# Kernel optimization log

Hardware: AMD Instinct MI355X
Metric: run time of the kernel (lower is better)

Reference implementation:

```python
import jax, jax.numpy as jnp
import numpy as np

CODEBOOK_SIZE = 8192
DIM = 64
B, N = 4, 4096


def setup_inputs() -> dict:
    key = jax.random.key(0)
    k1, k2 = jax.random.split(key)
    x = jax.random.normal(k1, (B, N, DIM), dtype=jnp.float32)
    node_mask = jnp.ones((B, N), dtype=jnp.float32)
    embed = jax.random.normal(k2, (CODEBOOK_SIZE, DIM), dtype=jnp.float32)
    return {"x": x, "node_mask": node_mask, "embed": embed}


def reference(x, node_mask, embed):
    # x: [B, N, D]; embed: [K, D]; node_mask: [B, N]
    b, n, d = x.shape
    k = embed.shape[0]
    flatten = x.reshape(-1, d)  # [B*N, D]
    dist = -(
        jnp.sum(flatten * flatten, axis=1, keepdims=True)
        - 2.0 * (flatten @ embed.T)
        + jnp.sum(embed * embed, axis=1)[None, :]
    )
    embed_ind = jnp.argmax(dist, axis=-1)  # [B*N] nearest-code assignment
    quantize = embed[embed_ind].reshape(b, n, d)  # codebook gather
    # masked one-hot stats (embed_onehot * node_mask), via segment_sum
    mask_flat = node_mask.reshape(-1)
    counts = jax.ops.segment_sum(mask_flat, embed_ind, num_segments=k)  # [K]
    avg_probs = counts / jnp.asarray(flatten.shape[0], dtype=x.dtype)
    perplexity = jnp.exp(-jnp.sum(avg_probs * jnp.log(avg_probs + 1e-10)))
    return quantize, embed_ind.reshape(b, n), perplexity
```

## Files before the change

### kernel.cpp

```cpp
#include <hip/hip_runtime.h>

typedef __attribute__((ext_vector_type(8))) short short8;
typedef __attribute__((ext_vector_type(4))) float f32x4;

#define ROWS 16384
#define DIM 64
#define NCODES 8192
#define MARGIN 0.008f
#define KT_FB 256
#define CTS_PER_BLOCK 32

#define WS_BEST   0
#define WS_COUNTS 131072
#define WS_ENH    163840
#define WS_ESWZ   196608
#define WS_NEED   2293760

__device__ __forceinline__ unsigned long long pack_score(float s, int idx) {
  unsigned u = __float_as_uint(s);
  u ^= (unsigned)((int)u >> 31) | 0x80000000u;
  return ((unsigned long long)u << 32) | (unsigned)(0xFFFF - idx);
}
__device__ __forceinline__ unsigned short bf16hi(float f) {
  unsigned u = __float_as_uint(f);
  return (unsigned short)((u + 0x7FFFu + ((u >> 16) & 1u)) >> 16);
}

__global__ void vq_enorm(const float* __restrict__ embed, float* __restrict__ enh) {
  int k = blockIdx.x * 256 + threadIdx.x;
  const float4* e4 = (const float4*)(embed + (size_t)k * DIM);
  float a = 0.f, b = 0.f, c = 0.f, d = 0.f;
#pragma unroll
  for (int i = 0; i < DIM / 4; ++i) {
    float4 v = e4[i];
    a = fmaf(v.x, v.x, a); b = fmaf(v.y, v.y, b);
    c = fmaf(v.z, v.z, c); d = fmaf(v.w, v.w, d);
  }
  enh[k] = 0.5f * ((a + b) + (c + d));
}

__global__ void vq_prep_e(const float* __restrict__ embed, short* __restrict__ eswz) {
  int u = blockIdx.x * 256 + threadIdx.x;
  int l = u & 63, kc = (u >> 6) & 1, ct = u >> 7;
  int code = ct * 16 + (l & 15);
  int kb = kc * 32 + (l >> 4) * 8;
  const float* er = embed + (size_t)code * DIM + kb;
  short8 h8, l8;
#pragma unroll
  for (int j = 0; j < 8; ++j) {
    float v = er[j];
    unsigned short h = bf16hi(v);
    float r = v - __uint_as_float((unsigned)h << 16);
    h8[j] = (short)h;
    l8[j] = (short)bf16hi(r);
  }
  short8* dst = (short8*)eswz;
  size_t frag = (size_t)(ct * 2 + kc) * 2;
  dst[(frag + 0) * 64 + l] = h8;
  dst[(frag + 1) * 64 + l] = l8;
}

__global__ __launch_bounds__(256, 4) void vq_screen(
    const float* __restrict__ x, const float* __restrict__ embed,
    const short* __restrict__ eswz, const float* __restrict__ enh,
    unsigned long long* __restrict__ best) {
  const int l = threadIdx.x & 63, wid = threadIdx.x >> 6;
  const int cl = l & 15, grp = l >> 4;
  const int row0 = blockIdx.x * 128 + wid * 32;
  const int ct0 = blockIdx.y * CTS_PER_BLOCK;

  short8 ahi[2][2], alo[2][2];
#pragma unroll
  for (int s = 0; s < 2; ++s) {
    const float* xr = x + (size_t)(row0 + s * 16 + cl) * DIM;
#pragma unroll
    for (int kc = 0; kc < 2; ++kc) {
      const int kb = kc * 32 + grp * 8;
#pragma unroll
      for (int j = 0; j < 8; ++j) {
        float v = xr[kb + j];
        unsigned short h = bf16hi(v);
        float r = v - __uint_as_float((unsigned)h << 16);
        ahi[s][kc][j] = (short)h;
        alo[s][kc][j] = (short)bf16hi(r);
      }
    }
  }

  const short8* eb = (const short8*)eswz;
  float bsc[2][4];
  int bidx[2][4];
#pragma unroll
  for (int s = 0; s < 2; ++s)
#pragma unroll
    for (int j = 0; j < 4; ++j) { bsc[s][j] = -3.4e38f; bidx[s][j] = 0; }

#pragma unroll 2
  for (int ct = ct0; ct < ct0 + CTS_PER_BLOCK; ++ct) {
    size_t f0 = (size_t)(ct * 2 + 0) * 128, f1 = (size_t)(ct * 2 + 1) * 128;
    short8 bh0 = eb[f0 + l], bl0 = eb[f0 + 64 + l];
    short8 bh1 = eb[f1 + l], bl1 = eb[f1 + 64 + l];
    float eh = enh[ct * 16 + cl];

    f32x4 accI = {-eh, -eh, -eh, -eh};
    f32x4 acc0 = accI, acc1 = accI;
    acc0 = __builtin_amdgcn_mfma_f32_16x16x32_bf16(ahi[0][0], bh0, acc0, 0, 0, 0);
    acc1 = __builtin_amdgcn_mfma_f32_16x16x32_bf16(ahi[1][0], bh0, acc1, 0, 0, 0);
    acc0 = __builtin_amdgcn_mfma_f32_16x16x32_bf16(alo[0][0], bh0, acc0, 0, 0, 0);
    acc1 = __builtin_amdgcn_mfma_f32_16x16x32_bf16(alo[1][0], bh0, acc1, 0, 0, 0);
    acc0 = __builtin_amdgcn_mfma_f32_16x16x32_bf16(ahi[0][0], bl0, acc0, 0, 0, 0);
    acc1 = __builtin_amdgcn_mfma_f32_16x16x32_bf16(ahi[1][0], bl0, acc1, 0, 0, 0);
    acc0 = __builtin_amdgcn_mfma_f32_16x16x32_bf16(ahi[0][1], bh1, acc0, 0, 0, 0);
    acc1 = __builtin_amdgcn_mfma_f32_16x16x32_bf16(ahi[1][1], bh1, acc1, 0, 0, 0);
    acc0 = __builtin_amdgcn_mfma_f32_16x16x32_bf16(alo[0][1], bh1, acc0, 0, 0, 0);
    acc1 = __builtin_amdgcn_mfma_f32_16x16x32_bf16(alo[1][1], bh1, acc1, 0, 0, 0);
    acc0 = __builtin_amdgcn_mfma_f32_16x16x32_bf16(ahi[0][1], bl1, acc0, 0, 0, 0);
    acc1 = __builtin_amdgcn_mfma_f32_16x16x32_bf16(ahi[1][1], bl1, acc1, 0, 0, 0);

    const int code = ct * 16 + cl;
#pragma unroll
    for (int j = 0; j < 4; ++j) {
      if (acc0[j] > bsc[0][j]) { bsc[0][j] = acc0[j]; bidx[0][j] = code; }
      if (acc1[j] > bsc[1][j]) { bsc[1][j] = acc1[j]; bidx[1][j] = code; }
    }
  }

  unsigned fmask = 0;
#pragma unroll
  for (int s = 0; s < 2; ++s)
#pragma unroll
    for (int j = 0; j < 4; ++j) {
      float m = bsc[s][j];
      m = fmaxf(m, __shfl_xor(m, 1));
      m = fmaxf(m, __shfl_xor(m, 2));
      m = fmaxf(m, __shfl_xor(m, 4));
      m = fmaxf(m, __shfl_xor(m, 8));
      if (bsc[s][j] >= m - MARGIN) fmask |= 1u << (s * 4 + j);
    }

  float exact[2][4];
#pragma unroll
  for (int s = 0; s < 2; ++s)
#pragma unroll
    for (int j = 0; j < 4; ++j) exact[s][j] = -3.4e38f;

  while (__any((int)(fmask != 0))) {
    const bool act = fmask != 0;
    const int sel = __ffs(fmask) - 1;
    int code = 0;
#pragma unroll
    for (int s = 0; s < 2; ++s)
#pragma unroll
      for (int j = 0; j < 4; ++j)
        code = (sel == s * 4 + j) ? bidx[s][j] : code;
    int row = act ? (row0 + (sel >> 2) * 16 + grp * 4 + (sel & 3)) : row0;
    if (!act) code = 0;
    const float4* xr = (const float4*)(x + (size_t)row * DIM);
    const float4* er = (const float4*)(embed + (size_t)code * DIM);
    float a0 = 0, a1 = 0, a2 = 0, a3 = 0, n0 = 0, n1 = 0, n2 = 0, n3 = 0;
#pragma unroll
    for (int i = 0; i < 16; ++i) {
      float4 xv = xr[i], ev = er[i];
      a0 = fmaf(xv.x, ev.x, a0); a1 = fmaf(xv.y, ev.y, a1);
      a2 = fmaf(xv.z, ev.z, a2); a3 = fmaf(xv.w, ev.w, a3);
      n0 = fmaf(ev.x, ev.x, n0); n1 = fmaf(ev.y, ev.y, n1);
      n2 = fmaf(ev.z, ev.z, n2); n3 = fmaf(ev.w, ev.w, n3);
    }
    float ex = ((a0 + a1) + (a2 + a3)) - 0.5f * ((n0 + n1) + (n2 + n3));
#pragma unroll
    for (int s = 0; s < 2; ++s)
#pragma unroll
      for (int j = 0; j < 4; ++j)
        exact[s][j] = (act && sel == s * 4 + j) ? ex : exact[s][j];
    fmask = act ? (fmask & (fmask - 1)) : 0u;
  }

#pragma unroll
  for (int s = 0; s < 2; ++s)
#pragma unroll
    for (int j = 0; j < 4; ++j) {
      unsigned long long pk = pack_score(exact[s][j], bidx[s][j]);
      unsigned long long o;
      o = __shfl_xor(pk, 1); pk = pk > o ? pk : o;
      o = __shfl_xor(pk, 2); pk = pk > o ? pk : o;
      o = __shfl_xor(pk, 4); pk = pk > o ? pk : o;
      o = __shfl_xor(pk, 8); pk = pk > o ? pk : o;
      if (cl == 0) atomicMax(&best[row0 + s * 16 + grp * 4 + j], pk);
    }
}

__global__ __launch_bounds__(256, 2) void vq_score_fb(
    const float* __restrict__ x, const float* __restrict__ embed,
    const float* __restrict__ enh, unsigned long long* __restrict__ best) {
  const int row = blockIdx.x * 256 + threadIdx.x;
  const int c0 = blockIdx.y * KT_FB;
  float4 xa[16];
  const float4* xg = (const float4*)(x + (size_t)row * DIM);
#pragma unroll
  for (int i = 0; i < 16; ++i) xa[i] = xg[i];
  float bs = -3.4e38f;
  int bc = 0;
#pragma unroll 2
  for (int c = c0; c < c0 + KT_FB; ++c) {
    const float4* e4 = (const float4*)(embed + (size_t)c * DIM);
    float a0 = 0.f, a1 = 0.f, a2 = 0.f, a3 = 0.f;
#pragma unroll
    for (int i = 0; i < 16; ++i) {
      float4 ev = e4[i];
      a0 = fmaf(xa[i].x, ev.x, a0); a1 = fmaf(xa[i].y, ev.y, a1);
      a2 = fmaf(xa[i].z, ev.z, a2); a3 = fmaf(xa[i].w, ev.w, a3);
    }
    float s = ((a0 + a1) + (a2 + a3)) - enh[c];
    if (s > bs) { bs = s; bc = c; }
  }
  atomicMax(&best[row], pack_score(bs, bc));
}

__global__ void vq_finalize(const unsigned long long* __restrict__ best,
                            const float* __restrict__ embed,
                            const float* __restrict__ node_mask,
                            float* __restrict__ quant,
                            float* __restrict__ out_idx,
                            float* __restrict__ counts) {
  int gid = blockIdx.x * 256 + threadIdx.x;
  int row = gid >> 6, d = gid & 63;
  unsigned long long p = best[row];
  int idx = 0xFFFF - (int)(p & 0xFFFFull);
  quant[gid] = embed[(size_t)idx * DIM + d];
  if (d == 0) {
    out_idx[row] = (float)idx;
    atomicAdd(&counts[idx], node_mask[row]);
  }
}

__global__ void vq_perplexity(const float* __restrict__ counts, float* __restrict__ out) {
  int tid = threadIdx.x;
  float acc = 0.f;
  for (int k = tid; k < NCODES; k += 256) {
    float p = counts[k] * (1.0f / (float)ROWS);
    acc += p * logf(p + 1e-10f);
  }
#pragma unroll
  for (int off = 32; off > 0; off >>= 1) acc += __shfl_down(acc, off);
  __shared__ float red[4];
  if ((tid & 63) == 0) red[tid >> 6] = acc;
  __syncthreads();
  if (tid == 0) out[0] = expf(-((red[0] + red[1]) + (red[2] + red[3])));
}

extern "C" void kernel_launch(void* const* d_in, const int* in_sizes, int n_in,
                              void* d_out, int out_size, void* d_ws, size_t ws_size,
                              hipStream_t stream) {
  const float* x = (const float*)d_in[0];
  const float* node_mask = (const float*)d_in[1];
  const float* embed = (const float*)d_in[2];

  float* out = (float*)d_out;
  float* quant = out;
  float* out_idx = out + (size_t)ROWS * DIM;
  float* out_ppl = out_idx + ROWS;

  unsigned long long* best = (unsigned long long*)((char*)d_ws + WS_BEST);
  float* counts = (float*)((char*)d_ws + WS_COUNTS);
  float* enh = (float*)((char*)d_ws + WS_ENH);
  short* eswz = (short*)((char*)d_ws + WS_ESWZ);

  hipMemsetAsync(d_ws, 0, WS_ENH, stream);
  vq_enorm<<<NCODES / 256, 256, 0, stream>>>(embed, enh);
  if (ws_size >= WS_NEED) {
    vq_prep_e<<<256, 256, 0, stream>>>(embed, eswz);
    vq_screen<<<dim3(ROWS / 128, NCODES / (CTS_PER_BLOCK * 16)), 256, 0, stream>>>(
        x, embed, eswz, enh, best);
  } else {
    vq_score_fb<<<dim3(ROWS / 256, NCODES / KT_FB), 256, 0, stream>>>(x, embed, enh, best);
  }
  vq_finalize<<<ROWS * DIM / 256, 256, 0, stream>>>(best, embed, node_mask, quant, out_idx, counts);
  vq_perplexity<<<1, 256, 0, stream>>>(counts, out_ppl);
}
```

Before: 117.9 us.

## Stage codebook fragments into LDS via global_load_lds and interleave MFMA chains

The screening kernel now copies each chunk of four code tiles of the pre-swizzled bf16 codebook into shared memory using the direct global-to-LDS load, so one copy is shared across the block's four waves instead of each wave loading it separately from global memory. It then processes two code tiles at once with four independent accumulator chains, giving the MFMA pipeline more independent work. The code-norm term is now subtracted after the matrix multiply rather than used as the initial accumulator. This adds two block barriers per chunk and does not overlap the loads with compute, so waves may stall waiting for the staging step. The prep kernel's fragment index expression is rewritten but computes the same layout.

```diff
diff --git a/kernel.cpp b/kernel.cpp
--- a/kernel.cpp
+++ b/kernel.cpp
@@ -9,6 +9,7 @@
 #define MARGIN 0.008f
 #define KT_FB 256
 #define CTS_PER_BLOCK 32
+#define CHUNK 4
 
 #define WS_BEST   0
 #define WS_COUNTS 131072
@@ -55,7 +56,7 @@
     l8[j] = (short)bf16hi(r);
   }
   short8* dst = (short8*)eswz;
-  size_t frag = (size_t)(ct * 2 + kc) * 2;
+  size_t frag = (size_t)ct * 4 + kc * 2;
   dst[(frag + 0) * 64 + l] = h8;
   dst[(frag + 1) * 64 + l] = l8;
 }
@@ -64,10 +65,13 @@
     const float* __restrict__ x, const float* __restrict__ embed,
     const short* __restrict__ eswz, const float* __restrict__ enh,
     unsigned long long* __restrict__ best) {
-  const int l = threadIdx.x & 63, wid = threadIdx.x >> 6;
+  const int t = threadIdx.x;
+  const int l = t & 63, wid = t >> 6;
   const int cl = l & 15, grp = l >> 4;
   const int row0 = blockIdx.x * 128 + wid * 32;
   const int ct0 = blockIdx.y * CTS_PER_BLOCK;
+
+  __shared__ short8 bstage[CHUNK * 4 * 64];
 
   short8 ahi[2][2], alo[2][2];
 #pragma unroll
@@ -87,7 +91,6 @@
     }
   }
 
-  const short8* eb = (const short8*)eswz;
   float bsc[2][4];
   int bidx[2][4];
 #pragma unroll
@@ -95,34 +98,71 @@
 #pragma unroll
     for (int j = 0; j < 4; ++j) { bsc[s][j] = -3.4e38f; bidx[s][j] = 0; }
 
-#pragma unroll 2
-  for (int ct = ct0; ct < ct0 + CTS_PER_BLOCK; ++ct) {
-    size_t f0 = (size_t)(ct * 2 + 0) * 128, f1 = (size_t)(ct * 2 + 1) * 128;
-    short8 bh0 = eb[f0 + l], bl0 = eb[f0 + 64 + l];
-    short8 bh1 = eb[f1 + l], bl1 = eb[f1 + 64 + l];
-    float eh = enh[ct * 16 + cl];
-
-    f32x4 accI = {-eh, -eh, -eh, -eh};
-    f32x4 acc0 = accI, acc1 = accI;
-    acc0 = __builtin_amdgcn_mfma_f32_16x16x32_bf16(ahi[0][0], bh0, acc0, 0, 0, 0);
-    acc1 = __builtin_amdgcn_mfma_f32_16x16x32_bf16(ahi[1][0], bh0, acc1, 0, 0, 0);
-    acc0 = __builtin_amdgcn_mfma_f32_16x16x32_bf16(alo[0][0], bh0, acc0, 0, 0, 0);
-    acc1 = __builtin_amdgcn_mfma_f32_16x16x32_bf16(alo[1][0], bh0, acc1, 0, 0, 0);
-    acc0 = __builtin_amdgcn_mfma_f32_16x16x32_bf16(ahi[0][0], bl0, acc0, 0, 0, 0);
-    acc1 = __builtin_amdgcn_mfma_f32_16x16x32_bf16(ahi[1][0], bl0, acc1, 0, 0, 0);
-    acc0 = __builtin_amdgcn_mfma_f32_16x16x32_bf16(ahi[0][1], bh1, acc0, 0, 0, 0);
-    acc1 = __builtin_amdgcn_mfma_f32_16x16x32_bf16(ahi[1][1], bh1, acc1, 0, 0, 0);
-    acc0 = __builtin_amdgcn_mfma_f32_16x16x32_bf16(alo[0][1], bh1, acc0, 0, 0, 0);
-    acc1 = __builtin_amdgcn_mfma_f32_16x16x32_bf16(alo[1][1], bh1, acc1, 0, 0, 0);
-    acc0 = __builtin_amdgcn_mfma_f32_16x16x32_bf16(ahi[0][1], bl1, acc0, 0, 0, 0);
-    acc1 = __builtin_amdgcn_mfma_f32_16x16x32_bf16(ahi[1][1], bl1, acc1, 0, 0, 0);
-
-    const int code = ct * 16 + cl;
-#pragma unroll
-    for (int j = 0; j < 4; ++j) {
-      if (acc0[j] > bsc[0][j]) { bsc[0][j] = acc0[j]; bidx[0][j] = code; }
-      if (acc1[j] > bsc[1][j]) { bsc[1][j] = acc1[j]; bidx[1][j] = code; }
-    }
+  for (int ch = 0; ch < CTS_PER_BLOCK / CHUNK; ++ch) {
+    const int cc = ct0 + ch * CHUNK;
+    {
+      const char* gb = (const char*)eswz + (size_t)cc * 4 * 1024;
+      char* lb = (char*)bstage;
+#pragma unroll
+      for (int i = 0; i < 4; ++i) {
+        const int e = i * 256 + t;
+        __builtin_amdgcn_global_load_lds(
+            (const __attribute__((address_space(1))) void*)(gb + (size_t)e * 16),
+            (__attribute__((address_space(3))) void*)(lb + e * 16), 16, 0, 0);
+      }
+    }
+    __syncthreads();
+
+#pragma unroll
+    for (int p = 0; p < 2; ++p) {
+      const int ctA = cc + 2 * p, ctB = ctA + 1;
+      const int ciA = 2 * p, ciB = 2 * p + 1;
+      float ehA = enh[ctA * 16 + cl];
+      float ehB = enh[ctB * 16 + cl];
+      short8 Ah0 = bstage[(ciA * 4 + 0) * 64 + l], Al0 = bstage[(ciA * 4 + 1) * 64 + l];
+      short8 Ah1 = bstage[(ciA * 4 + 2) * 64 + l], Al1 = bstage[(ciA * 4 + 3) * 64 + l];
+      short8 Bh0 = bstage[(ciB * 4 + 0) * 64 + l], Bl0 = bstage[(ciB * 4 + 1) * 64 + l];
+      short8 Bh1 = bstage[(ciB * 4 + 2) * 64 + l], Bl1 = bstage[(ciB * 4 + 3) * 64 + l];
+
+      f32x4 z = {0.f, 0.f, 0.f, 0.f};
+      f32x4 aA0 = z, aA1 = z, aB0 = z, aB1 = z;
+      aA0 = __builtin_amdgcn_mfma_f32_16x16x32_bf16(ahi[0][0], Ah0, aA0, 0, 0, 0);
+      aA1 = __builtin_amdgcn_mfma_f32_16x16x32_bf16(ahi[1][0], Ah0, aA1, 0, 0, 0);
+      aB0 = __builtin_amdgcn_mfma_f32_16x16x32_bf16(ahi[0][0], Bh0, aB0, 0, 0, 0);
+      aB1 = __builtin_amdgcn_mfma_f32_16x16x32_bf16(ahi[1][0], Bh0, aB1, 0, 0, 0);
+      aA0 = __builtin_amdgcn_mfma_f32_16x16x32_bf16(alo[0][0], Ah0, aA0, 0, 0, 0);
+      aA1 = __builtin_amdgcn_mfma_f32_16x16x32_bf16(alo[1][0], Ah0, aA1, 0, 0, 0);
+      aB0 = __builtin_amdgcn_mfma_f32_16x16x32_bf16(alo[0][0], Bh0, aB0, 0, 0, 0);
+      aB1 = __builtin_amdgcn_mfma_f32_16x16x32_bf16(alo[1][0], Bh0, aB1, 0, 0, 0);
+      aA0 = __builtin_amdgcn_mfma_f32_16x16x32_bf16(ahi[0][0], Al0, aA0, 0, 0, 0);
+      aA1 = __builtin_amdgcn_mfma_f32_16x16x32_bf16(ahi[1][0], Al0, aA1, 0, 0, 0);
+      aB0 = __builtin_amdgcn_mfma_f32_16x16x32_bf16(ahi[0][0], Bl0, aB0, 0, 0, 0);
+      aB1 = __builtin_amdgcn_mfma_f32_16x16x32_bf16(ahi[1][0], Bl0, aB1, 0, 0, 0);
+      aA0 = __builtin_amdgcn_mfma_f32_16x16x32_bf16(ahi[0][1], Ah1, aA0, 0, 0, 0);
+      aA1 = __builtin_amdgcn_mfma_f32_16x16x32_bf16(ahi[1][1], Ah1, aA1, 0, 0, 0);
+      aB0 = __builtin_amdgcn_mfma_f32_16x16x32_bf16(ahi[0][1], Bh1, aB0, 0, 0, 0);
+      aB1 = __builtin_amdgcn_mfma_f32_16x16x32_bf16(ahi[1][1], Bh1, aB1, 0, 0, 0);
+      aA0 = __builtin_amdgcn_mfma_f32_16x16x32_bf16(alo[0][1], Ah1, aA0, 0, 0, 0);
+      aA1 = __builtin_amdgcn_mfma_f32_16x16x32_bf16(alo[1][1], Ah1, aA1, 0, 0, 0);
+      aB0 = __builtin_amdgcn_mfma_f32_16x16x32_bf16(alo[0][1], Bh1, aB0, 0, 0, 0);
+      aB1 = __builtin_amdgcn_mfma_f32_16x16x32_bf16(alo[1][1], Bh1, aB1, 0, 0, 0);
+      aA0 = __builtin_amdgcn_mfma_f32_16x16x32_bf16(ahi[0][1], Al1, aA0, 0, 0, 0);
+      aA1 = __builtin_amdgcn_mfma_f32_16x16x32_bf16(ahi[1][1], Al1, aA1, 0, 0, 0);
+      aB0 = __builtin_amdgcn_mfma_f32_16x16x32_bf16(ahi[0][1], Bl1, aB0, 0, 0, 0);
+      aB1 = __builtin_amdgcn_mfma_f32_16x16x32_bf16(ahi[1][1], Bl1, aB1, 0, 0, 0);
+
+      const int codeA = ctA * 16 + cl, codeB = ctB * 16 + cl;
+#pragma unroll
+      for (int j = 0; j < 4; ++j) {
+        float sA0 = aA0[j] - ehA, sA1 = aA1[j] - ehA;
+        float sB0 = aB0[j] - ehB, sB1 = aB1[j] - ehB;
+        if (sA0 > bsc[0][j]) { bsc[0][j] = sA0; bidx[0][j] = codeA; }
+        if (sA1 > bsc[1][j]) { bsc[1][j] = sA1; bidx[1][j] = codeA; }
+        if (sB0 > bsc[0][j]) { bsc[0][j] = sB0; bidx[0][j] = codeB; }
+        if (sB1 > bsc[1][j]) { bsc[1][j] = sB1; bidx[1][j] = codeB; }
+      }
+    }
+    __syncthreads();
   }
 
   unsigned fmask = 0;
```

Measured after the change: 113.9 us. 3.4% less time.
